# Kernel optimization log

Hardware: AMD Instinct MI355X
Metric: run time of the kernel (lower is better)

The kernel has to match this reference:

```python
import jax, jax.numpy as jnp
import numpy as np

BS, GRID, A, CH = 32, 2704, 3, 85   # 52x52 YOLO grid, 3 anchors, 80 classes + 5
HW = 52
VDIM, H, SEL = 1024, 512, 32
EPS = 1e-8


def setup_inputs() -> dict:
    key = jax.random.key(0)
    ks = jax.random.split(key, 16)
    s = 0.02
    return {
        "boxes": jax.random.uniform(ks[0], (BS, GRID, A, CH), dtype=jnp.float32),
        "x_feat": jax.random.normal(ks[1], (BS, VDIM, HW, HW), dtype=jnp.float32),
        "tag_emb": jax.random.normal(ks[2], (BS, SEL, H), dtype=jnp.float32),
        "pos_emb": jax.random.normal(ks[3], (BS, SEL, H), dtype=jnp.float32),
        "lang": jax.random.normal(ks[4], (BS, H), dtype=jnp.float32),
        "W_vs": jax.random.normal(ks[5], (VDIM, H), dtype=jnp.float32) * s,
        "b_vs": jnp.zeros((H,), jnp.float32),
        "W_ts": jax.random.normal(ks[6], (H, H), dtype=jnp.float32) * s,
        "b_ts": jnp.zeros((H,), jnp.float32),
        "W_vs_pos": jax.random.normal(ks[7], (H, H), dtype=jnp.float32) * s,
        "b_vs_pos": jnp.zeros((H,), jnp.float32),
        "W_tag": jax.random.normal(ks[8], (H, H), dtype=jnp.float32) * s,
        "b_tag": jnp.zeros((H,), jnp.float32),
        "W_soft": jax.random.normal(ks[9], (H, 2), dtype=jnp.float32) * s,
        "b_soft": jnp.zeros((2,), jnp.float32),
    }


def reference(boxes, x_feat, tag_emb, pos_emb, lang,
              W_vs, b_vs, W_ts, b_ts, W_vs_pos, b_vs_pos,
              W_tag, b_tag, W_soft, b_soft):
    bs = boxes.shape[0]
    # --- topk grid selection on mean objectness (channel 4) ---
    score = jnp.mean(boxes, axis=2)[:, :, 4]                     # [bs, grid]
    _, idx = jax.lax.top_k(score, SEL)                           # [bs, SEL]
    # torch's scatter->masked_select recovers selected grids in ascending
    # index order (not topk-value order), so sort the indices.
    idx = jnp.sort(idx, axis=1)
    # gather selected boxes: [bs, SEL, A, CH]
    boxes_sel = jnp.take_along_axis(boxes, idx[:, :, None, None], axis=1)
    # gather selected visual features: [bs, SEL, VDIM]
    feat = x_feat.reshape(bs, VDIM, -1).transpose(0, 2, 1)       # [bs, grid, VDIM]
    i_sel = jnp.take_along_axis(feat, idx[:, :, None], axis=1)
    # --- gated multimodal fusion ---
    vis = i_sel @ W_vs + b_vs                                    # [bs, SEL, H]
    lang_e = (lang @ W_ts + b_ts)[:, None, :]                    # [bs, 1, H]
    logits = ((vis + tag_emb + pos_emb) @ W_soft + b_soft) / 0.03
    w = jax.nn.log_softmax(logits, axis=-1)                      # [bs, SEL, 2]
    vis2 = ((vis * w[..., 0:1]) @ W_vs_pos + b_vs_pos
            + (tag_emb * w[..., 1:2]) @ W_tag + b_tag
            + pos_emb)                                           # [bs, SEL, H]
    # --- head (eval): cosine similarity vs language, top-1 grid mask ---
    vn = vis2 / (jnp.linalg.norm(vis2, axis=-1, keepdims=True) + EPS)
    ln = lang_e / (jnp.linalg.norm(lang_e, axis=-1, keepdims=True) + EPS)
    sim = jnp.sum(vn * ln, axis=-1)                              # [bs, SEL]
    top_grid = jnp.argmax(sim, axis=1)                           # [bs]
    # --- get_boxes: gather top grid, xywh->xyxy, top-1 box by objectness ---
    sel = jnp.take_along_axis(boxes_sel, top_grid[:, None, None, None], axis=1)
    sel = jax.lax.stop_gradient(sel[:, 0])                       # [bs, A, CH] (.data in torch)
    x1 = sel[..., 0] - sel[..., 2] / 2
    y1 = sel[..., 1] - sel[..., 3] / 2
    x2 = x1 + sel[..., 2]
    y2 = y1 + sel[..., 3]
    bxyxy = jnp.concatenate(
        [jnp.stack([x1, y1, x2, y2], axis=-1), sel[..., 4:]], axis=-1)
    j = jnp.argmax(bxyxy[:, :, 4], axis=1)                       # [bs]
    box_pred = jnp.take_along_axis(bxyxy[:, :, :5], j[:, None, None], axis=1)
    return box_pred, sim
```

## Files before the change

kernel.cpp:

```cpp
#include <hip/hip_runtime.h>
#include <hip/hip_bf16.h>
#include <math.h>

#define BS   32
#define GRID_N 2704
#define A_N  3
#define CH   85
#define VDIM 1024
#define HDIM 512
#define SEL  32
#define ROWS (BS*SEL)

#define WS_ISEL  1024
#define WS_VIS   (WS_ISEL + ROWS*VDIM)
#define WS_VIS2  (WS_VIS + ROWS*HDIM)
#define WS_TOTAL_FLOATS (WS_VIS2 + ROWS*HDIM)

__global__ __launch_bounds__(256) void topk_kernel(const float* __restrict__ boxes,
                                                   int* __restrict__ idx_out) {
    __shared__ float sc[GRID_N];
    __shared__ int   selg[SEL];
    __shared__ float rbv[4];
    __shared__ int   rbi[4];
    int b = blockIdx.x, tid = threadIdx.x;
    for (int g = tid; g < GRID_N; g += 256) {
        const float* p = boxes + ((long)(b * GRID_N + g)) * (A_N * CH);
        sc[g] = (p[4] + p[CH + 4] + p[2 * CH + 4]) * (1.0f / 3.0f);
    }
    __syncthreads();
    for (int i = 0; i < SEL; ++i) {
        float bv = -3.4e38f; int bi = 0x7fffffff;
        for (int g = tid; g < GRID_N; g += 256) {
            float v = sc[g];
            if (v > bv || (v == bv && g < bi)) { bv = v; bi = g; }
        }
        for (int off = 32; off; off >>= 1) {
            float ov = __shfl_down(bv, off);
            int   oi = __shfl_down(bi, off);
            if (ov > bv || (ov == bv && oi < bi)) { bv = ov; bi = oi; }
        }
        int lane = tid & 63, wid = tid >> 6;
        if (lane == 0) { rbv[wid] = bv; rbi[wid] = bi; }
        __syncthreads();
        if (tid == 0) {
            float fv = rbv[0]; int fi = rbi[0];
            for (int w = 1; w < 4; ++w)
                if (rbv[w] > fv || (rbv[w] == fv && rbi[w] < fi)) { fv = rbv[w]; fi = rbi[w]; }
            selg[i] = fi;
            sc[fi] = -3.4e38f;
        }
        __syncthreads();
    }
    if (tid < SEL) {
        int my = selg[tid], rank = 0;
        for (int j = 0; j < SEL; ++j) rank += (selg[j] < my);
        idx_out[b * SEL + rank] = my;
    }
}

__global__ __launch_bounds__(256) void gather_kernel(const float* __restrict__ xf,
                                                     const int* __restrict__ idx,
                                                     float* __restrict__ isel) {
    int r = blockIdx.x;
    int b = r >> 5;
    int g = idx[r];
    const float* src = xf + (long)b * VDIM * GRID_N + g;
    float* dst = isel + (long)r * VDIM;
    #pragma unroll
    for (int j = 0; j < 4; ++j) {
        int v = threadIdx.x + j * 256;
        dst[v] = src[(long)v * GRID_N];
    }
}

#define KT 256
__global__ __launch_bounds__(256) void gemm1_kernel(const float* __restrict__ A,
                                                    const float* __restrict__ W,
                                                    const float* __restrict__ bias,
                                                    float* __restrict__ out) {
    __shared__ float As[KT][34];
    int tid = threadIdx.x;
    int bx = blockIdx.x, by = blockIdx.y;
    int ct = tid & 15, rt = tid >> 4;
    int c0 = by * 64 + ct * 4;
    int r0 = bx * 32 + rt * 2;
    int lrow = tid >> 3;
    int lk0  = (tid & 7) * 4;
    float acc[2][4] = {{0.f,0.f,0.f,0.f},{0.f,0.f,0.f,0.f}};
    for (int k0 = 0; k0 < VDIM; k0 += KT) {
        #pragma unroll
        for (int j = 0; j < 8; ++j) {
            int kk = lk0 + j * 32;
            float4 v = *(const float4*)&A[(long)(bx * 32 + lrow) * VDIM + k0 + kk];
            As[kk + 0][lrow] = v.x; As[kk + 1][lrow] = v.y;
            As[kk + 2][lrow] = v.z; As[kk + 3][lrow] = v.w;
        }
        __syncthreads();
        #pragma unroll 8
        for (int k = 0; k < KT; ++k) {
            float4 w = *(const float4*)&W[(long)(k0 + k) * HDIM + c0];
            float2 a = *(const float2*)&As[k][2 * rt];
            acc[0][0] += a.x * w.x; acc[0][1] += a.x * w.y;
            acc[0][2] += a.x * w.z; acc[0][3] += a.x * w.w;
            acc[1][0] += a.y * w.x; acc[1][1] += a.y * w.y;
            acc[1][2] += a.y * w.z; acc[1][3] += a.y * w.w;
        }
        __syncthreads();
    }
    float4 bv = *(const float4*)&bias[c0];
    #pragma unroll
    for (int i = 0; i < 2; ++i) {
        float4 o;
        o.x = acc[i][0] + bv.x; o.y = acc[i][1] + bv.y;
        o.z = acc[i][2] + bv.z; o.w = acc[i][3] + bv.w;
        *(float4*)&out[(long)(r0 + i) * HDIM + c0] = o;
    }
}

__global__ __launch_bounds__(256) void gemm2_kernel(const float* __restrict__ vis,
                                                    const float* __restrict__ tag,
                                                    const float* __restrict__ pos,
                                                    const float* __restrict__ Wsoft,
                                                    const float* __restrict__ bsoft,
                                                    const float* __restrict__ Wvp,
                                                    const float* __restrict__ Wtag,
                                                    const float* __restrict__ bvp,
                                                    const float* __restrict__ btag,
                                                    float* __restrict__ out) {
    __shared__ float As[KT][34];
    __shared__ float w0s[32];
    __shared__ float w1s[32];
    int tid = threadIdx.x;
    int bx = blockIdx.x, by = blockIdx.y;
    int ct = tid & 15, rt = tid >> 4;
    int c0 = by * 64 + ct * 4;
    int r0 = bx * 32 + rt * 2;
    int lrow = tid >> 3;
    int lk0  = (tid & 7) * 4;
    int grow = bx * 32 + lrow;

    {
        int sub = tid & 7;
        const float* vr = vis + (long)grow * HDIM + sub * 64;
        const float* tr = tag + (long)grow * HDIM + sub * 64;
        const float* pr = pos + (long)grow * HDIM + sub * 64;
        const float* wr = Wsoft + (sub * 64) * 2;
        float s0 = 0.f, s1 = 0.f;
        #pragma unroll
        for (int j = 0; j < 16; ++j) {
            float4 v = *(const float4*)&vr[j * 4];
            float4 t = *(const float4*)&tr[j * 4];
            float4 p = *(const float4*)&pr[j * 4];
            float4 wA = *(const float4*)&wr[j * 8];
            float4 wB = *(const float4*)&wr[j * 8 + 4];
            float e0 = v.x + t.x + p.x, e1 = v.y + t.y + p.y;
            float e2 = v.z + t.z + p.z, e3 = v.w + t.w + p.w;
            s0 += e0 * wA.x + e1 * wA.z + e2 * wB.x + e3 * wB.z;
            s1 += e0 * wA.y + e1 * wA.w + e2 * wB.y + e3 * wB.w;
        }
        s0 += __shfl_down(s0, 4, 8); s1 += __shfl_down(s1, 4, 8);
        s0 += __shfl_down(s0, 2, 8); s1 += __shfl_down(s1, 2, 8);
        s0 += __shfl_down(s0, 1, 8); s1 += __shfl_down(s1, 1, 8);
        if (sub == 0) {
            float l0 = (s0 + bsoft[0]) * (1.0f / 0.03f);
            float l1 = (s1 + bsoft[1]) * (1.0f / 0.03f);
            float m = fmaxf(l0, l1);
            float lse = m + logf(expf(l0 - m) + expf(l1 - m));
            w0s[lrow] = l0 - lse;
            w1s[lrow] = l1 - lse;
        }
    }
    __syncthreads();
    float sw0 = w0s[lrow], sw1 = w1s[lrow];

    float acc[2][4] = {{0.f,0.f,0.f,0.f},{0.f,0.f,0.f,0.f}};
    for (int k0 = 0; k0 < 2 * HDIM; k0 += KT) {
        #pragma unroll
        for (int j = 0; j < 8; ++j) {
            int kk = lk0 + j * 32;
            int kg = k0 + kk;
            float4 v; float s;
            if (kg < HDIM) {
                v = *(const float4*)&vis[(long)grow * HDIM + kg];
                s = sw0;
            } else {
                v = *(const float4*)&tag[(long)grow * HDIM + kg - HDIM];
                s = sw1;
            }
            As[kk + 0][lrow] = v.x * s; As[kk + 1][lrow] = v.y * s;
            As[kk + 2][lrow] = v.z * s; As[kk + 3][lrow] = v.w * s;
        }
        __syncthreads();
        const float* Wb = (k0 < HDIM) ? (Wvp + (long)k0 * HDIM)
                                      : (Wtag + (long)(k0 - HDIM) * HDIM);
        #pragma unroll 8
        for (int k = 0; k < KT; ++k) {
            float4 w = *(const float4*)&Wb[(long)k * HDIM + c0];
            float2 a = *(const float2*)&As[k][2 * rt];
            acc[0][0] += a.x * w.x; acc[0][1] += a.x * w.y;
            acc[0][2] += a.x * w.z; acc[0][3] += a.x * w.w;
            acc[1][0] += a.y * w.x; acc[1][1] += a.y * w.y;
            acc[1][2] += a.y * w.z; acc[1][3] += a.y * w.w;
        }
        __syncthreads();
    }
    float4 b1 = *(const float4*)&bvp[c0];
    float4 b2 = *(const float4*)&btag[c0];
    #pragma unroll
    for (int i = 0; i < 2; ++i) {
        int r = r0 + i;
        float4 p = *(const float4*)&pos[(long)r * HDIM + c0];
        float4 o;
        o.x = acc[i][0] + b1.x + b2.x + p.x;
        o.y = acc[i][1] + b1.y + b2.y + p.y;
        o.z = acc[i][2] + b1.z + b2.z + p.z;
        o.w = acc[i][3] + b1.w + b2.w + p.w;
        *(float4*)&out[(long)r * HDIM + c0] = o;
    }
}

__global__ __launch_bounds__(256) void final_kernel(const float* __restrict__ vis2,
                                                    const float* __restrict__ lang,
                                                    const float* __restrict__ Wts,
                                                    const float* __restrict__ bts,
                                                    const int* __restrict__ idx,
                                                    const float* __restrict__ boxes,
                                                    float* __restrict__ out) {
    __shared__ float ll[HDIM];
    __shared__ float lns[HDIM];
    __shared__ float red[4];
    __shared__ float sims[SEL];
    int b = blockIdx.x, tid = threadIdx.x;
    int lane = tid & 63, wid = tid >> 6;
    ll[tid]       = lang[b * HDIM + tid];
    ll[tid + 256] = lang[b * HDIM + tid + 256];
    __syncthreads();
    for (int h = tid; h < HDIM; h += 256) {
        float acc = bts[h];
        for (int k = 0; k < HDIM; ++k) acc += ll[k] * Wts[k * HDIM + h];
        lns[h] = acc;
    }
    __syncthreads();
    float s = lns[tid] * lns[tid] + lns[tid + 256] * lns[tid + 256];
    for (int off = 32; off; off >>= 1) s += __shfl_down(s, off);
    if (lane == 0) red[wid] = s;
    __syncthreads();
    float sscale;
    {
        float t = red[0] + red[1] + red[2] + red[3];
        sscale = 1.0f / (sqrtf(t) + 1e-8f);
    }
    for (int j = 0; j < 8; ++j) {
        int sl = wid + j * 4;
        const float* vr = vis2 + (long)(b * SEL + sl) * HDIM;
        int k = lane * 8;
        float ss = 0.f, dot = 0.f;
        #pragma unroll
        for (int t = 0; t < 8; ++t) {
            float v = vr[k + t];
            ss += v * v;
            dot += v * lns[k + t];
        }
        for (int off = 32; off; off >>= 1) {
            ss += __shfl_down(ss, off);
            dot += __shfl_down(dot, off);
        }
        if (lane == 0) {
            float sim = dot * sscale / (sqrtf(ss) + 1e-8f);
            out[BS * 5 + b * SEL + sl] = sim;
            sims[sl] = sim;
        }
    }
    __syncthreads();
    if (tid == 0) {
        int bsi = 0; float bvv = sims[0];
        for (int sl = 1; sl < SEL; ++sl)
            if (sims[sl] > bvv) { bvv = sims[sl]; bsi = sl; }
        int g = idx[b * SEL + bsi];
        const float* bb = boxes + ((long)(b * GRID_N + g)) * A_N * CH;
        float o0 = bb[4], o1 = bb[CH + 4], o2 = bb[2 * CH + 4];
        int j = 0; float ov = o0;
        if (o1 > ov) { ov = o1; j = 1; }
        if (o2 > ov) { ov = o2; j = 2; }
        const float* sb = bb + j * CH;
        float x = sb[0], y = sb[1], w = sb[2], h = sb[3];
        float x1 = x - w * 0.5f, y1 = y - h * 0.5f;
        out[b * 5 + 0] = x1;
        out[b * 5 + 1] = y1;
        out[b * 5 + 2] = x1 + w;
        out[b * 5 + 3] = y1 + h;
        out[b * 5 + 4] = sb[4];
    }
}

extern "C" void kernel_launch(void* const* d_in, const int* in_sizes, int n_in,
                              void* d_out, int out_size, void* d_ws, size_t ws_size,
                              hipStream_t stream) {
    const float* boxes    = (const float*)d_in[0];
    const float* x_feat   = (const float*)d_in[1];
    const float* tag_emb  = (const float*)d_in[2];
    const float* pos_emb  = (const float*)d_in[3];
    const float* lang     = (const float*)d_in[4];
    const float* W_vs     = (const float*)d_in[5];
    const float* b_vs     = (const float*)d_in[6];
    const float* W_ts     = (const float*)d_in[7];
    const float* b_ts     = (const float*)d_in[8];
    const float* W_vs_pos = (const float*)d_in[9];
    const float* b_vs_pos = (const float*)d_in[10];
    const float* W_tag    = (const float*)d_in[11];
    const float* b_tag    = (const float*)d_in[12];
    const float* W_soft   = (const float*)d_in[13];
    const float* b_soft   = (const float*)d_in[14];
    float* out = (float*)d_out;

    if (ws_size < (size_t)WS_TOTAL_FLOATS * sizeof(float)) return;

    float* wsf   = (float*)d_ws;
    int*   wsidx = (int*)d_ws;
    float* isel  = wsf + WS_ISEL;
    float* vis   = wsf + WS_VIS;
    float* vis2  = wsf + WS_VIS2;

    topk_kernel<<<BS, 256, 0, stream>>>(boxes, wsidx);
    gather_kernel<<<ROWS, 256, 0, stream>>>(x_feat, wsidx, isel);
    gemm1_kernel<<<dim3(32, 8), 256, 0, stream>>>(isel, W_vs, b_vs, vis);
    gemm2_kernel<<<dim3(32, 8), 256, 0, stream>>>(vis, tag_emb, pos_emb, W_soft, b_soft,
                                                  W_vs_pos, W_tag, b_vs_pos, b_tag, vis2);
    final_kernel<<<BS, 256, 0, stream>>>(vis2, lang, W_ts, b_ts, wsidx, boxes, out);
}
```

Baseline: 755.3 us.

## Split objectness scoring into wide kernel and double-buffer GEMM A tiles

Moves the per-grid mean objectness computation out of the 32-block topk kernel into a separate fully parallel kernel writing scores to workspace, so the strided box reads are spread over many blocks. Both GEMM kernels switch to a smaller k-tile with two shared-memory buffers and register prefetch of the next A tile, overlapping global loads with FMA work. This adds an extra launch and workspace round trip for scores, and the smaller tile raises the number of synchronizations.

```diff
diff --git a/kernel.cpp b/kernel.cpp
--- a/kernel.cpp
+++ b/kernel.cpp
@@ -11,22 +11,27 @@
 #define SEL  32
 #define ROWS (BS*SEL)
 
-#define WS_ISEL  1024
-#define WS_VIS   (WS_ISEL + ROWS*VDIM)
-#define WS_VIS2  (WS_VIS + ROWS*HDIM)
-#define WS_TOTAL_FLOATS (WS_VIS2 + ROWS*HDIM)
-
-__global__ __launch_bounds__(256) void topk_kernel(const float* __restrict__ boxes,
+#define WS_ISEL   1024
+#define WS_VIS    (WS_ISEL + ROWS*VDIM)
+#define WS_VIS2   (WS_VIS + ROWS*HDIM)
+#define WS_SCORE  (WS_VIS2 + ROWS*HDIM)
+#define WS_TOTAL_FLOATS (WS_SCORE + BS*GRID_N)
+
+__global__ __launch_bounds__(256) void score_kernel(const float* __restrict__ boxes,
+                                                    float* __restrict__ score) {
+    int t = blockIdx.x * 256 + threadIdx.x;
+    const float* p = boxes + (long)t * (A_N * CH);
+    score[t] = (p[4] + p[CH + 4] + p[2 * CH + 4]) * (1.0f / 3.0f);
+}
+
+__global__ __launch_bounds__(256) void topk_kernel(const float* __restrict__ score,
                                                    int* __restrict__ idx_out) {
     __shared__ float sc[GRID_N];
     __shared__ int   selg[SEL];
     __shared__ float rbv[4];
     __shared__ int   rbi[4];
     int b = blockIdx.x, tid = threadIdx.x;
-    for (int g = tid; g < GRID_N; g += 256) {
-        const float* p = boxes + ((long)(b * GRID_N + g)) * (A_N * CH);
-        sc[g] = (p[4] + p[CH + 4] + p[2 * CH + 4]) * (1.0f / 3.0f);
-    }
+    for (int g = tid; g < GRID_N; g += 256) sc[g] = score[b * GRID_N + g];
     __syncthreads();
     for (int i = 0; i < SEL; ++i) {
         float bv = -3.4e38f; int bi = 0x7fffffff;
@@ -73,12 +78,13 @@
     }
 }
 
-#define KT 256
+#define KT 128
+#define LSTR 33
 __global__ __launch_bounds__(256) void gemm1_kernel(const float* __restrict__ A,
                                                     const float* __restrict__ W,
                                                     const float* __restrict__ bias,
                                                     float* __restrict__ out) {
-    __shared__ float As[KT][34];
+    __shared__ float As[2][KT][LSTR];
     int tid = threadIdx.x;
     int bx = blockIdx.x, by = blockIdx.y;
     int ct = tid & 15, rt = tid >> 4;
@@ -86,24 +92,42 @@
     int r0 = bx * 32 + rt * 2;
     int lrow = tid >> 3;
     int lk0  = (tid & 7) * 4;
+    const float* arow = A + (long)(bx * 32 + lrow) * VDIM;
     float acc[2][4] = {{0.f,0.f,0.f,0.f},{0.f,0.f,0.f,0.f}};
-    for (int k0 = 0; k0 < VDIM; k0 += KT) {
-        #pragma unroll
-        for (int j = 0; j < 8; ++j) {
-            int kk = lk0 + j * 32;
-            float4 v = *(const float4*)&A[(long)(bx * 32 + lrow) * VDIM + k0 + kk];
-            As[kk + 0][lrow] = v.x; As[kk + 1][lrow] = v.y;
-            As[kk + 2][lrow] = v.z; As[kk + 3][lrow] = v.w;
-        }
-        __syncthreads();
+    float4 pre[4];
+    #pragma unroll
+    for (int j = 0; j < 4; ++j) pre[j] = *(const float4*)&arow[lk0 + j * 32];
+    #pragma unroll
+    for (int j = 0; j < 4; ++j) {
+        int kk = lk0 + j * 32;
+        As[0][kk + 0][lrow] = pre[j].x; As[0][kk + 1][lrow] = pre[j].y;
+        As[0][kk + 2][lrow] = pre[j].z; As[0][kk + 3][lrow] = pre[j].w;
+    }
+    __syncthreads();
+    #pragma unroll
+    for (int t = 0; t < VDIM / KT; ++t) {
+        int buf = t & 1;
+        if (t < VDIM / KT - 1) {
+            #pragma unroll
+            for (int j = 0; j < 4; ++j)
+                pre[j] = *(const float4*)&arow[(t + 1) * KT + lk0 + j * 32];
+        }
         #pragma unroll 8
         for (int k = 0; k < KT; ++k) {
-            float4 w = *(const float4*)&W[(long)(k0 + k) * HDIM + c0];
-            float2 a = *(const float2*)&As[k][2 * rt];
+            float4 w = *(const float4*)&W[(long)(t * KT + k) * HDIM + c0];
+            float2 a = *(const float2*)&As[buf][k][2 * rt];
             acc[0][0] += a.x * w.x; acc[0][1] += a.x * w.y;
             acc[0][2] += a.x * w.z; acc[0][3] += a.x * w.w;
             acc[1][0] += a.y * w.x; acc[1][1] += a.y * w.y;
             acc[1][2] += a.y * w.z; acc[1][3] += a.y * w.w;
+        }
+        if (t < VDIM / KT - 1) {
+            #pragma unroll
+            for (int j = 0; j < 4; ++j) {
+                int kk = lk0 + j * 32;
+                As[buf ^ 1][kk + 0][lrow] = pre[j].x; As[buf ^ 1][kk + 1][lrow] = pre[j].y;
+                As[buf ^ 1][kk + 2][lrow] = pre[j].z; As[buf ^ 1][kk + 3][lrow] = pre[j].w;
+            }
         }
         __syncthreads();
     }
@@ -127,7 +151,7 @@
                                                     const float* __restrict__ bvp,
                                                     const float* __restrict__ btag,
                                                     float* __restrict__ out) {
-    __shared__ float As[KT][34];
+    __shared__ float As[2][KT][LSTR];
     __shared__ float w0s[32];
     __shared__ float w1s[32];
     int tid = threadIdx.x;
@@ -138,11 +162,13 @@
     int lrow = tid >> 3;
     int lk0  = (tid & 7) * 4;
     int grow = bx * 32 + lrow;
+    const float* vrow = vis + (long)grow * HDIM;
+    const float* trow = tag + (long)grow * HDIM;
 
     {
         int sub = tid & 7;
-        const float* vr = vis + (long)grow * HDIM + sub * 64;
-        const float* tr = tag + (long)grow * HDIM + sub * 64;
+        const float* vr = vrow + sub * 64;
+        const float* tr = trow + sub * 64;
         const float* pr = pos + (long)grow * HDIM + sub * 64;
         const float* wr = Wsoft + (sub * 64) * 2;
         float s0 = 0.f, s1 = 0.f;
@@ -173,34 +199,48 @@
     __syncthreads();
     float sw0 = w0s[lrow], sw1 = w1s[lrow];
 
+    const int NT = (2 * HDIM) / KT;
     float acc[2][4] = {{0.f,0.f,0.f,0.f},{0.f,0.f,0.f,0.f}};
-    for (int k0 = 0; k0 < 2 * HDIM; k0 += KT) {
-        #pragma unroll
-        for (int j = 0; j < 8; ++j) {
-            int kk = lk0 + j * 32;
-            int kg = k0 + kk;
-            float4 v; float s;
-            if (kg < HDIM) {
-                v = *(const float4*)&vis[(long)grow * HDIM + kg];
-                s = sw0;
-            } else {
-                v = *(const float4*)&tag[(long)grow * HDIM + kg - HDIM];
-                s = sw1;
-            }
-            As[kk + 0][lrow] = v.x * s; As[kk + 1][lrow] = v.y * s;
-            As[kk + 2][lrow] = v.z * s; As[kk + 3][lrow] = v.w * s;
-        }
-        __syncthreads();
-        const float* Wb = (k0 < HDIM) ? (Wvp + (long)k0 * HDIM)
-                                      : (Wtag + (long)(k0 - HDIM) * HDIM);
+    float4 pre[4];
+    #pragma unroll
+    for (int j = 0; j < 4; ++j) pre[j] = *(const float4*)&vrow[lk0 + j * 32];
+    #pragma unroll
+    for (int j = 0; j < 4; ++j) {
+        int kk = lk0 + j * 32;
+        As[0][kk + 0][lrow] = pre[j].x * sw0; As[0][kk + 1][lrow] = pre[j].y * sw0;
+        As[0][kk + 2][lrow] = pre[j].z * sw0; As[0][kk + 3][lrow] = pre[j].w * sw0;
+    }
+    __syncthreads();
+    #pragma unroll
+    for (int t = 0; t < NT; ++t) {
+        int buf = t & 1;
+        float sn = 0.f;
+        if (t < NT - 1) {
+            int kg = (t + 1) * KT;
+            const float* srow = (kg < HDIM) ? (vrow + kg) : (trow + kg - HDIM);
+            sn = (kg < HDIM) ? sw0 : sw1;
+            #pragma unroll
+            for (int j = 0; j < 4; ++j)
+                pre[j] = *(const float4*)&srow[lk0 + j * 32];
+        }
+        const float* Wb = (t * KT < HDIM) ? (Wvp + (long)(t * KT) * HDIM)
+                                          : (Wtag + (long)(t * KT - HDIM) * HDIM);
         #pragma unroll 8
         for (int k = 0; k < KT; ++k) {
             float4 w = *(const float4*)&Wb[(long)k * HDIM + c0];
-            float2 a = *(const float2*)&As[k][2 * rt];
+            float2 a = *(const float2*)&As[buf][k][2 * rt];
             acc[0][0] += a.x * w.x; acc[0][1] += a.x * w.y;
             acc[0][2] += a.x * w.z; acc[0][3] += a.x * w.w;
             acc[1][0] += a.y * w.x; acc[1][1] += a.y * w.y;
             acc[1][2] += a.y * w.z; acc[1][3] += a.y * w.w;
+        }
+        if (t < NT - 1) {
+            #pragma unroll
+            for (int j = 0; j < 4; ++j) {
+                int kk = lk0 + j * 32;
+                As[buf ^ 1][kk + 0][lrow] = pre[j].x * sn; As[buf ^ 1][kk + 1][lrow] = pre[j].y * sn;
+                As[buf ^ 1][kk + 2][lrow] = pre[j].z * sn; As[buf ^ 1][kk + 3][lrow] = pre[j].w * sn;
+            }
         }
         __syncthreads();
     }
@@ -320,8 +360,10 @@
     float* isel  = wsf + WS_ISEL;
     float* vis   = wsf + WS_VIS;
     float* vis2  = wsf + WS_VIS2;
-
-    topk_kernel<<<BS, 256, 0, stream>>>(boxes, wsidx);
+    float* score = wsf + WS_SCORE;
+
+    score_kernel<<<(BS * GRID_N) / 256, 256, 0, stream>>>(boxes, score);
+    topk_kernel<<<BS, 256, 0, stream>>>(score, wsidx);
     gather_kernel<<<ROWS, 256, 0, stream>>>(x_feat, wsidx, isel);
     gemm1_kernel<<<dim3(32, 8), 256, 0, stream>>>(isel, W_vs, b_vs, vis);
     gemm2_kernel<<<dim3(32, 8), 256, 0, stream>>>(vis, tag_emb, pos_emb, W_soft, b_soft,
```

Measured after the change: 748.0 us. About the same (-1.0%).
